# Optimization experiments

Measured on AMD Instinct MI355X. Metric: run time of the kernel, lower is better.

The kernel has to match this reference:

```python
import jax, jax.numpy as jnp
import numpy as np

EPS = 1e-6

def layernorm2d(x, w, b):
    # normalize over channel dim (axis=1) of NCHW, per spatial location
    mu = jnp.mean(x, axis=1, keepdims=True)
    var = jnp.var(x, axis=1, keepdims=True)
    xn = (x - mu) * jax.lax.rsqrt(var + EPS)
    return xn * w[None, :, None, None] + b[None, :, None, None]

def conv1x1(x, w, b):
    # x: (B,C,H,W), w: (O,C), b: (O,)
    return jnp.einsum('bchw,oc->bohw', x, w) + b[None, :, None, None]

def setup_inputs() -> dict:
    key = jax.random.key(0)
    ks = jax.random.split(key, 9)
    B, C, H, W = 8, 256, 128, 128
    scale = 1.0 / np.sqrt(C)
    return {
        'x': jax.random.normal(ks[0], (B, C, H, W), jnp.float32),
        'norm_w': jnp.ones((C,), jnp.float32),
        'norm_b': jnp.zeros((C,), jnp.float32),
        'wq': jax.random.normal(ks[1], (C, C), jnp.float32) * scale,
        'bq': jnp.zeros((C,), jnp.float32),
        'wk': jax.random.normal(ks[2], (C, C), jnp.float32) * scale,
        'bk': jnp.zeros((C,), jnp.float32),
        'wv': jax.random.normal(ks[3], (C, C), jnp.float32) * scale,
        'bv': jnp.zeros((C,), jnp.float32),
        'beta': jax.random.normal(ks[4], (1, C, 1, 1), jnp.float32) * 0.1,
    }

def reference(x, norm_w, norm_b, wq, bq, wk, bk, wv, bv, beta):
    C = x.shape[1]
    scale = C ** (-0.5)
    xn = layernorm2d(x, norm_w, norm_b)
    Q = conv1x1(xn, wq, bq)          # (B,C,H,W)
    K = conv1x1(xn, wk, bk)          # (B,C,H,W)
    V = conv1x1(x, wv, bv)           # (B,C,H,W)
    # axial (per-row) attention: logits (B,H,W,W)
    attn = jnp.einsum('bchw,bchv->bhwv', Q, K) * scale
    A = jax.nn.softmax(attn, axis=-1)
    F_self = jnp.einsum('bhwv,bchv->bchw', A, V)
    return x + F_self * beta
```

## Files before the change

### kernel.cpp

```cpp
#include <hip/hip_runtime.h>
#include <hip/hip_bf16.h>

typedef short short8 __attribute__((ext_vector_type(8)));
typedef float f32x4 __attribute__((ext_vector_type(4)));

#define XN 0
#define AT 0
#define YTH 32768
#define GB 65536
#define SUMO 65536
#define SQO 69632
#define NW 73728
#define NB 74752
#define UU 75776
#define MUO 76800
#define RSO 77312
#define UDO 77824
#define LDS_BYTES 78336

__device__ inline unsigned short cvtbf(float f){
  unsigned int x = __float_as_uint(f);
  x += 0x7fffu + ((x >> 16) & 1u);
  return (unsigned short)(x >> 16);
}
__device__ inline float bf2f(unsigned short u){ return __uint_as_float(((unsigned int)u) << 16); }
__device__ inline unsigned int pk2(float a, float b){ return (unsigned int)cvtbf(a) | ((unsigned int)cvtbf(b) << 16); }

__global__ void __launch_bounds__(256) setup_kernel(
    const float* __restrict__ wq, const float* __restrict__ bq,
    const float* __restrict__ wk, const float* __restrict__ wvw,
    unsigned short* __restrict__ Mbf, unsigned short* __restrict__ wvbf, float* __restrict__ u){
  int t = threadIdx.x;
  int c1b = blockIdx.x * 4;
  float acc[4] = {0.f,0.f,0.f,0.f};
  for (int o = 0; o < 256; ++o){
    float wkv = wk[o*256 + t];
    #pragma unroll
    for (int i = 0; i < 4; ++i) acc[i] = fmaf(wq[o*256 + c1b + i], wkv, acc[i]);
  }
  #pragma unroll
  for (int i = 0; i < 4; ++i){
    Mbf[(c1b+i)*256 + t] = cvtbf(acc[i]);
    wvbf[(c1b+i)*256 + t] = cvtbf(wvw[(c1b+i)*256 + t]);
  }
  if (blockIdx.x == 0){
    float a2 = 0.f;
    for (int o = 0; o < 256; ++o) a2 = fmaf(wk[o*256 + t], bq[o], a2);
    u[t] = a2;
  }
}

__global__ void __launch_bounds__(512, 4) fused_kernel(
    const float* __restrict__ x, const float* __restrict__ nw, const float* __restrict__ nbp,
    const float* __restrict__ bvv, const float* __restrict__ beta,
    const unsigned short* __restrict__ Mbf, const unsigned short* __restrict__ wvbf,
    const float* __restrict__ u, float* __restrict__ out){
  extern __shared__ char smem[];
  const int t = threadIdx.x;
  const int lane = t & 63, wv8 = t >> 6;
  const int g = lane >> 4, li = lane & 15;
  const int blk = blockIdx.x;
  const int b = blk >> 7, h = blk & 127;
  const size_t base = (size_t)b*4194304 + (size_t)h*128;

  if (t < 256){
    ((float*)(smem + NW))[t] = nw[t];
    ((float*)(smem + NB))[t] = nbp[t];
    ((float*)(smem + UU))[t] = u[t];
  }

  const int w2 = t & 63, s = t >> 6;
  unsigned int xp[32];
  {
    const float* xw = x + base + (size_t)(s*32)*16384 + 2*w2;
    float sm0 = 0.f, sq0 = 0.f, sm1 = 0.f, sq1 = 0.f;
    #pragma unroll
    for (int j = 0; j < 32; ++j){
      float2 v = *(const float2*)(xw + (size_t)j*16384);
      sm0 += v.x; sq0 = fmaf(v.x, v.x, sq0);
      sm1 += v.y; sq1 = fmaf(v.y, v.y, sq1);
      xp[j] = pk2(v.x, v.y);
    }
    ((float*)(smem + SUMO))[s*128 + 2*w2]     = sm0;
    ((float*)(smem + SUMO))[s*128 + 2*w2 + 1] = sm1;
    ((float*)(smem + SQO))[s*128 + 2*w2]      = sq0;
    ((float*)(smem + SQO))[s*128 + 2*w2 + 1]  = sq1;
  }
  __syncthreads();
  if (t < 128){
    float sm = 0.f, sq = 0.f;
    #pragma unroll
    for (int q = 0; q < 8; ++q){ sm += ((float*)(smem+SUMO))[q*128+t]; sq += ((float*)(smem+SQO))[q*128+t]; }
    float mu = sm * (1.f/256.f);
    float var = sq * (1.f/256.f) - mu*mu;
    ((float*)(smem+MUO))[t] = mu;
    ((float*)(smem+RSO))[t] = rsqrtf(var + 1e-6f);
  }
  __syncthreads();

  {
    float ud[2] = {0.f, 0.f};
    #pragma unroll
    for (int r = 0; r < 2; ++r){
      int w = 2*w2 + r;
      float mu = ((float*)(smem+MUO))[w], rs = ((float*)(smem+RSO))[w];
      #pragma unroll
      for (int i = 0; i < 4; ++i){
        int c0 = s*32 + i*8;
        short8 o8;
        #pragma unroll
        for (int j = 0; j < 8; ++j){
          int c = c0 + j;
          unsigned int p = xp[i*8 + j];
          float xv = bf2f((unsigned short)(r ? (p >> 16) : (p & 0xffffu)));
          float nv = (xv - mu)*rs*((float*)(smem+NW))[c] + ((float*)(smem+NB))[c];
          ud[r] = fmaf(((float*)(smem+UU))[c], nv, ud[r]);
          o8[j] = (short)cvtbf(nv);
        }
        *(short8*)(smem + XN + w*512 + ((2*c0) ^ ((w&31)<<4))) = o8;
      }
    }
    __syncthreads();
    ((float*)(smem+SUMO))[s*128 + 2*w2]     = ud[0];
    ((float*)(smem+SUMO))[s*128 + 2*w2 + 1] = ud[1];
  }
  __syncthreads();
  if (t < 128){
    float ud = 0.f;
    #pragma unroll
    for (int q = 0; q < 8; ++q) ud += ((float*)(smem+SUMO))[q*128+t];
    ((float*)(smem+UDO))[t] = ud;
  }
  __syncthreads();

  f32x4 Sacc[8];
  #pragma unroll
  for (int vt = 0; vt < 8; ++vt){
    int vb = vt*16 + g*4;
    #pragma unroll
    for (int r = 0; r < 4; ++r) Sacc[vt][r] = ((float*)(smem+UDO))[vb + r];
  }
  const int ot = wv8 >> 2, vp = wv8 & 3;
  const int wt = wv8;
  short8 mpre[4];
  #pragma unroll
  for (int kk = 0; kk < 4; ++kk)
    mpre[kk] = *(const short8*)(Mbf + (ot*16 + li)*256 + kk*32 + g*8);
  #pragma unroll
  for (int k8 = 0; k8 < 8; ++k8){
    f32x4 Ga[2] = {{0.f,0.f,0.f,0.f},{0.f,0.f,0.f,0.f}};
    const int o = k8*32 + ot*16 + li;
    short8 mnext[4];
    __builtin_amdgcn_s_setprio(1);
    #pragma unroll
    for (int kk = 0; kk < 8; ++kk){
      short8 afr = (kk < 4) ? mpre[kk]
                 : *(const short8*)(Mbf + o*256 + kk*32 + g*8);
      if (kk < 4 && k8 < 7){
        mnext[kk] = *(const short8*)(Mbf + ((k8+1)*32 + ot*16 + li)*256 + kk*32 + g*8);
      }
      #pragma unroll
      for (int j = 0; j < 2; ++j){
        int v = (vp*2 + j)*16 + li;
        short8 bfr = *(const short8*)(smem + XN + v*512 + ((2*(kk*32 + g*8)) ^ ((v&31)<<4)));
        Ga[j] = __builtin_amdgcn_mfma_f32_16x16x32_bf16(afr, bfr, Ga[j], 0, 0, 0);
      }
    }
    __builtin_amdgcn_s_setprio(0);
    #pragma unroll
    for (int kk = 0; kk < 4; ++kk) mpre[kk] = mnext[kk];
    __syncthreads();
    #pragma unroll
    for (int j = 0; j < 2; ++j){
      int v = (vp*2 + j)*16 + li;
      int ob = ot*16 + g*4;
      uint2 p; p.x = pk2(Ga[j][0], Ga[j][1]); p.y = pk2(Ga[j][2], Ga[j][3]);
      *(uint2*)(smem + GB + v*64 + ((2*ob) ^ ((v&3)<<4))) = p;
    }
    __syncthreads();
    {
      int ww = wt*16 + li;
      short8 bfr = *(const short8*)(smem + XN + ww*512 + ((2*(k8*32 + g*8)) ^ ((ww&31)<<4)));
      __builtin_amdgcn_s_setprio(1);
      #pragma unroll
      for (int vt = 0; vt < 8; ++vt){
        int v = vt*16 + li;
        short8 afr = *(const short8*)(smem + GB + v*64 + ((16*g) ^ ((v&3)<<4)));
        Sacc[vt] = __builtin_amdgcn_mfma_f32_16x16x32_bf16(afr, bfr, Sacc[vt], 0, 0, 0);
      }
      __builtin_amdgcn_s_setprio(0);
    }
  }
  __syncthreads();

  float4 xe[2][2][2];
  #pragma unroll
  for (int kb = 0; kb < 2; ++kb)
    #pragma unroll
    for (int ci = 0; ci < 2; ++ci){
      int c = (wv8*2 + ci)*16 + li;
      const float* xs = x + base + (size_t)c*16384 + (kb*32 + g*8);
      xe[kb][ci][0] = *(const float4*)xs;
      xe[kb][ci][1] = *(const float4*)(xs + 4);
    }

  float mx = -3.4e38f;
  #pragma unroll
  for (int vt = 0; vt < 8; ++vt)
    #pragma unroll
    for (int r = 0; r < 4; ++r){ float sv = Sacc[vt][r]*0.0625f; Sacc[vt][r] = sv; mx = fmaxf(mx, sv); }
  mx = fmaxf(mx, __shfl_xor(mx, 16));
  mx = fmaxf(mx, __shfl_xor(mx, 32));
  float sum = 0.f;
  #pragma unroll
  for (int vt = 0; vt < 8; ++vt)
    #pragma unroll
    for (int r = 0; r < 4; ++r){ float p = exp2f((Sacc[vt][r]-mx)*1.44269504f); Sacc[vt][r] = p; sum += p; }
  sum += __shfl_xor(sum, 16);
  sum += __shfl_xor(sum, 32);
  float inv = 1.f / sum;
  {
    int ww = wt*16 + li;
    #pragma unroll
    for (int vt = 0; vt < 8; ++vt){
      uint2 p; p.x = pk2(Sacc[vt][0]*inv, Sacc[vt][1]*inv); p.y = pk2(Sacc[vt][2]*inv, Sacc[vt][3]*inv);
      int vb = vt*16 + g*4;
      *(uint2*)(smem + AT + ww*256 + ((2*vb) ^ ((ww&15)<<4))) = p;
    }
  }
  __syncthreads();

  f32x4 Yacc[2][8];
  #pragma unroll
  for (int ci = 0; ci < 2; ++ci)
    #pragma unroll
    for (int w2i = 0; w2i < 8; ++w2i) Yacc[ci][w2i] = (f32x4){0.f,0.f,0.f,0.f};
  #pragma unroll
  for (int kk = 0; kk < 4; ++kk){
    short8 afr[2];
    #pragma unroll
    for (int ci = 0; ci < 2; ++ci){
      const float4 f0 = xe[kk&1][ci][0];
      const float4 f1 = xe[kk&1][ci][1];
      short8 a;
      a[0]=(short)cvtbf(f0.x); a[1]=(short)cvtbf(f0.y); a[2]=(short)cvtbf(f0.z); a[3]=(short)cvtbf(f0.w);
      a[4]=(short)cvtbf(f1.x); a[5]=(short)cvtbf(f1.y); a[6]=(short)cvtbf(f1.z); a[7]=(short)cvtbf(f1.w);
      afr[ci] = a;
    }
    if (kk < 2){
      #pragma unroll
      for (int ci = 0; ci < 2; ++ci){
        int c = (wv8*2 + ci)*16 + li;
        const float* xs = x + base + (size_t)c*16384 + ((kk+2)*32 + g*8);
        xe[kk&1][ci][0] = *(const float4*)xs;
        xe[kk&1][ci][1] = *(const float4*)(xs + 4);
      }
    }
    __builtin_amdgcn_s_setprio(1);
    #pragma unroll
    for (int w2i = 0; w2i < 8; ++w2i){
      int ww = w2i*16 + li;
      short8 bfr = *(const short8*)(smem + AT + ww*256 + ((2*(kk*32 + g*8)) ^ ((ww&15)<<4)));
      #pragma unroll
      for (int ci = 0; ci < 2; ++ci)
        Yacc[ci][w2i] = __builtin_amdgcn_mfma_f32_16x16x32_bf16(afr[ci], bfr, Yacc[ci][w2i], 0, 0, 0);
    }
    __builtin_amdgcn_s_setprio(0);
  }

  f32x4 Facc[2][8];
  #pragma unroll
  for (int oi = 0; oi < 2; ++oi)
    #pragma unroll
    for (int w2i = 0; w2i < 8; ++w2i) Facc[oi][w2i] = (f32x4){0.f,0.f,0.f,0.f};
  #pragma unroll
  for (int half = 0; half < 2; ++half){
    if ((wv8 >> 2) == half){
      #pragma unroll
      for (int ci = 0; ci < 2; ++ci){
        int cb = ((wv8 & 3)*2 + ci)*16 + g*4;
        #pragma unroll
        for (int w2i = 0; w2i < 8; ++w2i){
          int ww = w2i*16 + li;
          uint2 p; p.x = pk2(Yacc[ci][w2i][0], Yacc[ci][w2i][1]); p.y = pk2(Yacc[ci][w2i][2], Yacc[ci][w2i][3]);
          *(uint2*)(smem + YTH + ww*256 + ((2*cb) ^ ((ww&15)<<4))) = p;
        }
      }
    }
    __syncthreads();
    #pragma unroll
    for (int kk = 0; kk < 4; ++kk){
      short8 afr[2];
      #pragma unroll
      for (int oi = 0; oi < 2; ++oi){
        int o = (wv8*2 + oi)*16 + li;
        afr[oi] = *(const short8*)(wvbf + o*256 + half*128 + kk*32 + g*8);
      }
      __builtin_amdgcn_s_setprio(1);
      #pragma unroll
      for (int w2i = 0; w2i < 8; ++w2i){
        int ww = w2i*16 + li;
        short8 bfr = *(const short8*)(smem + YTH + ww*256 + ((2*(kk*32 + g*8)) ^ ((ww&15)<<4)));
        #pragma unroll
        for (int oi = 0; oi < 2; ++oi)
          Facc[oi][w2i] = __builtin_amdgcn_mfma_f32_16x16x32_bf16(afr[oi], bfr, Facc[oi][w2i], 0, 0, 0);
      }
      __builtin_amdgcn_s_setprio(0);
    }
    __syncthreads();
  }

  #pragma unroll
  for (int oi = 0; oi < 2; ++oi){
    #pragma unroll
    for (int r = 0; r < 4; ++r){
      int o = (wv8*2 + oi)*16 + g*4 + r;
      float bvo = bvv[o], bto = beta[o];
      #pragma unroll
      for (int w2i = 0; w2i < 8; ++w2i){
        int ww = w2i*16 + li;
        size_t idx = base + (size_t)o*16384 + (size_t)ww;
        out[idx] = x[idx] + (Facc[oi][w2i][r] + bvo)*bto;
      }
    }
  }
}

extern "C" void kernel_launch(void* const* d_in, const int* in_sizes, int n_in,
                              void* d_out, int out_size, void* d_ws, size_t ws_size,
                              hipStream_t stream) {
  (void)in_sizes; (void)n_in; (void)out_size; (void)ws_size;
  const float* x      = (const float*)d_in[0];
  const float* norm_w = (const float*)d_in[1];
  const float* norm_b = (const float*)d_in[2];
  const float* wq     = (const float*)d_in[3];
  const float* bq     = (const float*)d_in[4];
  const float* wk     = (const float*)d_in[5];
  const float* wvw    = (const float*)d_in[7];
  const float* bvv    = (const float*)d_in[8];
  const float* beta   = (const float*)d_in[9];
  float* out = (float*)d_out;

  unsigned short* Mbf  = (unsigned short*)d_ws;
  unsigned short* wvbf = (unsigned short*)((char*)d_ws + 131072);
  float* u             = (float*)((char*)d_ws + 262144);

  static bool attr_set = false;
  if (!attr_set) {
    (void)hipFuncSetAttribute((const void*)fused_kernel,
                              hipFuncAttributeMaxDynamicSharedMemorySize, LDS_BYTES);
    attr_set = true;
  }

  setup_kernel<<<64, 256, 0, stream>>>(wq, bq, wk, wvw, Mbf, wvbf, u);
  fused_kernel<<<1024, 512, LDS_BYTES, stream>>>(x, norm_w, norm_b, bvv, beta, Mbf, wvbf, u, out);
}
```

Before: 209.4 us.

## Use fp8 for attention-V matmul, reuse register x, and stage output through LDS

The attention-times-V MFMA now runs in fp8. Both the bf16 copy of x already held in registers and the normalized attention weights are packed to fp8 in LDS, so x is no longer reloaded from global memory for that step. The residual add uses the same register-held bf16 x instead of re-reading fp32 x. Output tiles are staged in LDS as bf16 so the stores can be written as coalesced float2 runs. The software prefetch of the fused weight matrix is dropped and the LDS layout is reorganised; fp8 attention/V and a bf16 residual reduce accuracy.

```diff
diff --git a/kernel.cpp b/kernel.cpp
--- a/kernel.cpp
+++ b/kernel.cpp
@@ -5,18 +5,22 @@
 typedef float f32x4 __attribute__((ext_vector_type(4)));
 
 #define XN 0
-#define AT 0
-#define YTH 32768
+#define XS 0
+#define AT 49152
+#define YTH 0
+#define FLD 0
 #define GB 65536
-#define SUMO 65536
-#define SQO 69632
-#define NW 73728
-#define NB 74752
-#define UU 75776
-#define MUO 76800
-#define RSO 77312
-#define UDO 77824
-#define LDS_BYTES 78336
+#define NW 65536
+#define NB 66560
+#define UU 67584
+#define MUO 68608
+#define RSO 69120
+#define UDO 69632
+#define SUMO 73728
+#define SQO 77824
+#define BV 73728
+#define BT 74752
+#define LDS_BYTES 81920
 
 __device__ inline unsigned short cvtbf(float f){
   unsigned int x = __float_as_uint(f);
@@ -25,6 +29,8 @@
 }
 __device__ inline float bf2f(unsigned short u){ return __uint_as_float(((unsigned int)u) << 16); }
 __device__ inline unsigned int pk2(float a, float b){ return (unsigned int)cvtbf(a) | ((unsigned int)cvtbf(b) << 16); }
+__device__ inline float lo16(unsigned int v){ return bf2f((unsigned short)(v & 0xffffu)); }
+__device__ inline float hi16(unsigned int v){ return bf2f((unsigned short)(v >> 16)); }
 
 __global__ void __launch_bounds__(256) setup_kernel(
     const float* __restrict__ wq, const float* __restrict__ bq,
@@ -59,8 +65,7 @@
   const int t = threadIdx.x;
   const int lane = t & 63, wv8 = t >> 6;
   const int g = lane >> 4, li = lane & 15;
-  const int blk = blockIdx.x;
-  const int b = blk >> 7, h = blk & 127;
+  const int b = blockIdx.x >> 7, h = blockIdx.x & 127;
   const size_t base = (size_t)b*4194304 + (size_t)h*128;
 
   if (t < 256){
@@ -133,6 +138,10 @@
   }
   __syncthreads();
 
+  if (t < 256){
+    ((float*)(smem + BV))[t] = bvv[t];
+    ((float*)(smem + BT))[t] = beta[t];
+  }
   f32x4 Sacc[8];
   #pragma unroll
   for (int vt = 0; vt < 8; ++vt){
@@ -142,23 +151,14 @@
   }
   const int ot = wv8 >> 2, vp = wv8 & 3;
   const int wt = wv8;
-  short8 mpre[4];
-  #pragma unroll
-  for (int kk = 0; kk < 4; ++kk)
-    mpre[kk] = *(const short8*)(Mbf + (ot*16 + li)*256 + kk*32 + g*8);
   #pragma unroll
   for (int k8 = 0; k8 < 8; ++k8){
     f32x4 Ga[2] = {{0.f,0.f,0.f,0.f},{0.f,0.f,0.f,0.f}};
     const int o = k8*32 + ot*16 + li;
-    short8 mnext[4];
     __builtin_amdgcn_s_setprio(1);
     #pragma unroll
     for (int kk = 0; kk < 8; ++kk){
-      short8 afr = (kk < 4) ? mpre[kk]
-                 : *(const short8*)(Mbf + o*256 + kk*32 + g*8);
-      if (kk < 4 && k8 < 7){
-        mnext[kk] = *(const short8*)(Mbf + ((k8+1)*32 + ot*16 + li)*256 + kk*32 + g*8);
-      }
+      short8 afr = *(const short8*)(Mbf + o*256 + kk*32 + g*8);
       #pragma unroll
       for (int j = 0; j < 2; ++j){
         int v = (vp*2 + j)*16 + li;
@@ -167,8 +167,6 @@
       }
     }
     __builtin_amdgcn_s_setprio(0);
-    #pragma unroll
-    for (int kk = 0; kk < 4; ++kk) mpre[kk] = mnext[kk];
     __syncthreads();
     #pragma unroll
     for (int j = 0; j < 2; ++j){
@@ -193,16 +191,12 @@
   }
   __syncthreads();
 
-  float4 xe[2][2][2];
-  #pragma unroll
-  for (int kb = 0; kb < 2; ++kb)
-    #pragma unroll
-    for (int ci = 0; ci < 2; ++ci){
-      int c = (wv8*2 + ci)*16 + li;
-      const float* xs = x + base + (size_t)c*16384 + (kb*32 + g*8);
-      xe[kb][ci][0] = *(const float4*)xs;
-      xe[kb][ci][1] = *(const float4*)(xs + 4);
-    }
+  #pragma unroll
+  for (int j = 0; j < 32; ++j){
+    int c = s*32 + j;
+    int pr = __builtin_amdgcn_cvt_pk_fp8_f32(lo16(xp[j]), hi16(xp[j]), 0, false);
+    *(unsigned short*)(smem + XS + c*128 + ((2*w2) ^ ((c&15)<<3))) = (unsigned short)pr;
+  }
 
   float mx = -3.4e38f;
   #pragma unroll
@@ -223,9 +217,9 @@
     int ww = wt*16 + li;
     #pragma unroll
     for (int vt = 0; vt < 8; ++vt){
-      uint2 p; p.x = pk2(Sacc[vt][0]*inv, Sacc[vt][1]*inv); p.y = pk2(Sacc[vt][2]*inv, Sacc[vt][3]*inv);
-      int vb = vt*16 + g*4;
-      *(uint2*)(smem + AT + ww*256 + ((2*vb) ^ ((ww&15)<<4))) = p;
+      int pr = __builtin_amdgcn_cvt_pk_fp8_f32(Sacc[vt][0]*inv, Sacc[vt][1]*inv, 0, false);
+      pr = __builtin_amdgcn_cvt_pk_fp8_f32(Sacc[vt][2]*inv, Sacc[vt][3]*inv, pr, true);
+      *(unsigned int*)(smem + AT + ww*128 + ((vt*16 + g*4) ^ ((ww&15)<<3))) = (unsigned int)pr;
     }
   }
   __syncthreads();
@@ -237,36 +231,24 @@
     for (int w2i = 0; w2i < 8; ++w2i) Yacc[ci][w2i] = (f32x4){0.f,0.f,0.f,0.f};
   #pragma unroll
   for (int kk = 0; kk < 4; ++kk){
-    short8 afr[2];
+    long af[2];
     #pragma unroll
     for (int ci = 0; ci < 2; ++ci){
-      const float4 f0 = xe[kk&1][ci][0];
-      const float4 f1 = xe[kk&1][ci][1];
-      short8 a;
-      a[0]=(short)cvtbf(f0.x); a[1]=(short)cvtbf(f0.y); a[2]=(short)cvtbf(f0.z); a[3]=(short)cvtbf(f0.w);
-      a[4]=(short)cvtbf(f1.x); a[5]=(short)cvtbf(f1.y); a[6]=(short)cvtbf(f1.z); a[7]=(short)cvtbf(f1.w);
-      afr[ci] = a;
-    }
-    if (kk < 2){
-      #pragma unroll
-      for (int ci = 0; ci < 2; ++ci){
-        int c = (wv8*2 + ci)*16 + li;
-        const float* xs = x + base + (size_t)c*16384 + ((kk+2)*32 + g*8);
-        xe[kk&1][ci][0] = *(const float4*)xs;
-        xe[kk&1][ci][1] = *(const float4*)(xs + 4);
-      }
+      int c = (wv8*2 + ci)*16 + li;
+      af[ci] = *(const long*)(smem + XS + c*128 + ((kk*32 + g*8) ^ ((c&15)<<3)));
     }
     __builtin_amdgcn_s_setprio(1);
     #pragma unroll
     for (int w2i = 0; w2i < 8; ++w2i){
       int ww = w2i*16 + li;
-      short8 bfr = *(const short8*)(smem + AT + ww*256 + ((2*(kk*32 + g*8)) ^ ((ww&15)<<4)));
+      long bf = *(const long*)(smem + AT + ww*128 + ((kk*32 + g*8) ^ ((ww&15)<<3)));
       #pragma unroll
       for (int ci = 0; ci < 2; ++ci)
-        Yacc[ci][w2i] = __builtin_amdgcn_mfma_f32_16x16x32_bf16(afr[ci], bfr, Yacc[ci][w2i], 0, 0, 0);
+        Yacc[ci][w2i] = __builtin_amdgcn_mfma_f32_16x16x32_fp8_fp8(af[ci], bf, Yacc[ci][w2i], 0, 0, 0);
     }
     __builtin_amdgcn_s_setprio(0);
   }
+  __syncthreads();
 
   f32x4 Facc[2][8];
   #pragma unroll
@@ -313,16 +295,34 @@
   #pragma unroll
   for (int oi = 0; oi < 2; ++oi){
     #pragma unroll
-    for (int r = 0; r < 4; ++r){
-      int o = (wv8*2 + oi)*16 + g*4 + r;
-      float bvo = bvv[o], bto = beta[o];
+    for (int rp = 0; rp < 2; ++rp){
+      int o0 = (wv8*2 + oi)*16 + g*4 + 2*rp;
+      int orow = o0 >> 1;
+      float bv0 = ((float*)(smem+BV))[o0],   bt0 = ((float*)(smem+BT))[o0];
+      float bv1 = ((float*)(smem+BV))[o0+1], bt1 = ((float*)(smem+BT))[o0+1];
       #pragma unroll
       for (int w2i = 0; w2i < 8; ++w2i){
-        int ww = w2i*16 + li;
-        size_t idx = base + (size_t)o*16384 + (size_t)ww;
-        out[idx] = x[idx] + (Facc[oi][w2i][r] + bvo)*bto;
-      }
-    }
+        int w = w2i*16 + li;
+        float f0 = (Facc[oi][w2i][2*rp]   + bv0)*bt0;
+        float f1 = (Facc[oi][w2i][2*rp+1] + bv1)*bt1;
+        *(unsigned int*)(smem + FLD + orow*512 + ((4*w) ^ ((orow&7)<<4))) = pk2(f0, f1);
+      }
+    }
+  }
+  __syncthreads();
+
+  #pragma unroll
+  for (int j = 0; j < 16; ++j){
+    int crow = s*16 + j;
+    uint2 u2 = *(const uint2*)(smem + FLD + crow*512 + ((8*w2) ^ ((crow&7)<<4)));
+    float2 o0, o1;
+    o0.x = lo16(xp[2*j])   + lo16(u2.x);
+    o0.y = hi16(xp[2*j])   + lo16(u2.y);
+    o1.x = lo16(xp[2*j+1]) + hi16(u2.x);
+    o1.y = hi16(xp[2*j+1]) + hi16(u2.y);
+    size_t c0 = (size_t)(s*32 + 2*j);
+    *(float2*)(out + base + c0*16384 + 2*w2)       = o0;
+    *(float2*)(out + base + (c0+1)*16384 + 2*w2)   = o1;
   }
 }
 
```

New measurement: 302.3 us. +44.4%, slower.
